# Optimization experiments

Hardware: AMD Instinct MI355X
Metric: run time of the kernel (lower is better)

The kernel has to match this reference:

```python
import jax, jax.numpy as jnp
import numpy as np

VIS_DIM, TXT_DIM, HID = 2048, 1024, 1024


def setup_inputs() -> dict:
    key = jax.random.key(0)
    ks = jax.random.split(key, 8)
    def lin(kw, kb, fan_in, fan_out):
        bound = 1.0 / np.sqrt(fan_in)
        W = jax.random.uniform(kw, (fan_out, fan_in), jnp.float32, -bound, bound)
        b = jax.random.uniform(kb, (fan_out,), jnp.float32, -bound, bound)
        return W, b
    Wv, bv = lin(ks[0], ks[1], VIS_DIM, HID)
    Wt, bt = lin(ks[2], ks[3], TXT_DIM, HID)
    Wa, ba = lin(ks[4], ks[5], HID, 1)
    return {
        "visual_features": jax.random.normal(ks[6], (128, 256, VIS_DIM), jnp.float32),
        "text_features": jax.random.normal(ks[7], (128, TXT_DIM), jnp.float32),
        "Wv": Wv, "bv": bv, "Wt": Wt, "bt": bt, "Wa": Wa, "ba": ba,
    }


def reference(visual_features, text_features, Wv, bv, Wt, bt, Wa, ba):
    # v: (B, R, H); t: (B, 1, H) broadcast over regions
    v = jnp.einsum("brd,hd->brh", visual_features, Wv) + bv
    t = (text_features @ Wt.T + bt)[:, None, :]
    combined = jnp.tanh(v + t)                       # (B, R, H)
    scores = jnp.einsum("brh,h->br", combined, Wa[0]) + ba[0]  # (B, R)
    attention_weights = jax.nn.softmax(scores, axis=1)
    attended = jnp.einsum("br,brd->bd", attention_weights, visual_features)
    return attended, attention_weights
```

## Files before the change

### kernel.cpp

```cpp
#include <hip/hip_runtime.h>
#include <hip/hip_bf16.h>

#define VIS_DIM 2048
#define TXT_DIM 1024
#define HID     1024
#define NB      128
#define NR      256
#define M_TOT   (NB*NR)

#define N_ATILES 8192
#define N_TILES  8448
#define TILE_B   16384
#define WS_SCORES_OFF ((size_t)N_TILES * TILE_B)
#define WS_NEED (WS_SCORES_OFF + 131072 + 524288)

typedef __attribute__((ext_vector_type(4))) float  f32x4;
typedef __attribute__((ext_vector_type(8))) short  short8;
typedef __attribute__((ext_vector_type(4))) unsigned short u16x4;

static __device__ __forceinline__ unsigned short f2bf(float f) {
    union { __hip_bfloat16 h; unsigned short u; } c;
    c.h = __float2bfloat16(f);
    return c.u;
}

static __device__ __forceinline__ float tanh_fast(float x) {
    float xc = fminf(fmaxf(x, -15.f), 15.f);
    float e  = __expf(2.f * xc);
    return (e - 1.f) / (e + 1.f);
}

__global__ void init_ws(float* __restrict__ scores, float* __restrict__ tbuf,
                        const float* __restrict__ bt) {
    int i = blockIdx.x * 256 + threadIdx.x;
    if (i < M_TOT) scores[i] = 0.f;
    tbuf[i] = bt[i & (HID - 1)];
}

__global__ __launch_bounds__(256) void prepass(const float* __restrict__ A,
                                               const float* __restrict__ Bv,
                                               unsigned short* __restrict__ w16) {
    const int t   = blockIdx.x;
    const int tid = threadIdx.x;
    const int mb  = (t < N_ATILES ? t : t - N_ATILES) >> 5;
    const int kt  = t & 31;
    const float* src = (t < N_ATILES ? A : Bv) + (size_t)mb * 128 * VIS_DIM + kt * 64;
    unsigned short* dst = w16 + (size_t)t * (TILE_B / 2);
    #pragma unroll
    for (int i = 0; i < 4; ++i) {
        int si = i * 256 + tid;
        int row = si >> 3, slot = si & 7;
        const float* p = src + (size_t)row * VIS_DIM + slot * 8;
        f32x4 lo = *(const f32x4*)p;
        f32x4 hi = *(const f32x4*)(p + 4);
        short8 v;
        v[0] = (short)f2bf(lo.x); v[1] = (short)f2bf(lo.y);
        v[2] = (short)f2bf(lo.z); v[3] = (short)f2bf(lo.w);
        v[4] = (short)f2bf(hi.x); v[5] = (short)f2bf(hi.y);
        v[6] = (short)f2bf(hi.z); v[7] = (short)f2bf(hi.w);
        *(short8*)(dst + row * 64 + ((slot ^ (row & 7)) << 3)) = v;
    }
}

__global__ __launch_bounds__(256) void gemm_text(const float* __restrict__ text,
                                                 const float* __restrict__ Wt,
                                                 float* __restrict__ tbuf) {
    __shared__ float As[128][33];
    __shared__ float Bs[32][33];
    const int n0  = blockIdx.x * 32;
    const int k0  = blockIdx.y * 256;
    const int tid = threadIdx.x;
    const int tm  = tid >> 3;
    const int tn  = tid & 7;
    float acc[4][4] = {};
    for (int kt = 0; kt < 8; ++kt) {
        const int k = k0 + kt * 32;
        {
            int row = tid >> 1, off = (tid & 1) * 16;
            const float* src = text + row * TXT_DIM + k + off;
            #pragma unroll
            for (int j = 0; j < 4; ++j) {
                f32x4 v = *(const f32x4*)(src + j * 4);
                As[row][off + j*4 + 0] = v.x; As[row][off + j*4 + 1] = v.y;
                As[row][off + j*4 + 2] = v.z; As[row][off + j*4 + 3] = v.w;
            }
        }
        {
            int row = tid >> 3, off = (tid & 7) * 4;
            f32x4 v = *(const f32x4*)(Wt + (size_t)(n0 + row) * TXT_DIM + k + off);
            Bs[row][off + 0] = v.x; Bs[row][off + 1] = v.y;
            Bs[row][off + 2] = v.z; Bs[row][off + 3] = v.w;
        }
        __syncthreads();
        #pragma unroll
        for (int kk = 0; kk < 32; ++kk) {
            float a[4], b[4];
            #pragma unroll
            for (int i = 0; i < 4; ++i) a[i] = As[tm*4 + i][kk];
            #pragma unroll
            for (int j = 0; j < 4; ++j) b[j] = Bs[tn*4 + j][kk];
            #pragma unroll
            for (int i = 0; i < 4; ++i)
                #pragma unroll
                for (int j = 0; j < 4; ++j) acc[i][j] += a[i] * b[j];
        }
        __syncthreads();
    }
    #pragma unroll
    for (int i = 0; i < 4; ++i)
        #pragma unroll
        for (int j = 0; j < 4; ++j)
            atomicAdd(&tbuf[(tm*4 + i) * HID + n0 + tn*4 + j], acc[i][j]);
}

static __device__ __forceinline__ int toff(int row, int kElem) {
    return row * 128 + ((((kElem >> 3) & 7) ^ (row & 7)) << 4);
}

__global__ __launch_bounds__(256, 3) void gemm_fast(
        const unsigned short* __restrict__ w16,
        const float* __restrict__ bv,
        const float* __restrict__ wa,
        const float* __restrict__ tbuf,
        float* __restrict__ scores) {
    __shared__ __align__(16) char lds[32768];

    const int wg   = blockIdx.x;
    const int xcd  = wg & 7;
    const int loc  = wg >> 3;
    const int mb   = xcd * 32 + (loc >> 3);
    const int nb   = loc & 7;
    const int brow = mb * 128;
    const int bcol = nb * 128;

    const int tid  = threadIdx.x;
    const int lane = tid & 63;
    const int wid  = tid >> 6;
    const int wr   = wid >> 1, wc = wid & 1;
    const int l    = lane & 15, g = lane >> 4;

    const char* Abase = (const char*)w16 + (size_t)(mb * 32) * TILE_B;
    const char* Bbase = (const char*)w16 + (size_t)(N_ATILES + nb * 32) * TILE_B;
    const int uoff = wid * 4096;

    f32x4 acc[4][4] = {};

    for (int kt = 0; kt < 32; ++kt) {
        const char* At = Abase + (size_t)kt * TILE_B;
        const char* Bt = Bbase + (size_t)kt * TILE_B;
        #pragma unroll
        for (int j = 0; j < 4; ++j) {
            const int off = uoff + j * 1024;
            __builtin_amdgcn_global_load_lds(
                (const __attribute__((address_space(1))) float*)(At + off + lane * 16),
                (__attribute__((address_space(3))) float*)(lds + off), 16, 0, 0);
            __builtin_amdgcn_global_load_lds(
                (const __attribute__((address_space(1))) float*)(Bt + off + lane * 16),
                (__attribute__((address_space(3))) float*)(lds + 16384 + off), 16, 0, 0);
        }
        __syncthreads();
        #pragma unroll
        for (int s = 0; s < 2; ++s) {
            short8 af[4], bf[4];
            const int kE = s * 32 + g * 8;
            #pragma unroll
            for (int m = 0; m < 4; ++m)
                af[m] = *(const short8*)(lds + toff(wr*64 + m*16 + l, kE));
            #pragma unroll
            for (int n = 0; n < 4; ++n)
                bf[n] = *(const short8*)(lds + 16384 + toff(wc*64 + n*16 + l, kE));
            #pragma unroll
            for (int m = 0; m < 4; ++m)
                #pragma unroll
                for (int n = 0; n < 4; ++n)
                    acc[m][n] = __builtin_amdgcn_mfma_f32_16x16x32_bf16(
                        af[m], bf[n], acc[m][n], 0, 0, 0);
        }
        __syncthreads();
    }

    const int b = brow >> 8;
    float wa_c[4], bvt_c[4];
    #pragma unroll
    for (int n = 0; n < 4; ++n) {
        int col = bcol + wc * 64 + n * 16 + l;
        wa_c[n]  = wa[col];
        bvt_c[n] = bv[col] + tbuf[b * HID + col];
    }
    #pragma unroll
    for (int m = 0; m < 4; ++m) {
        float p0 = 0.f, p1 = 0.f, p2 = 0.f, p3 = 0.f;
        #pragma unroll
        for (int n = 0; n < 4; ++n) {
            f32x4 v = acc[m][n];
            p0 += wa_c[n] * tanh_fast(v.x + bvt_c[n]);
            p1 += wa_c[n] * tanh_fast(v.y + bvt_c[n]);
            p2 += wa_c[n] * tanh_fast(v.z + bvt_c[n]);
            p3 += wa_c[n] * tanh_fast(v.w + bvt_c[n]);
        }
        #pragma unroll
        for (int d = 1; d < 16; d <<= 1) {
            p0 += __shfl_xor(p0, d); p1 += __shfl_xor(p1, d);
            p2 += __shfl_xor(p2, d); p3 += __shfl_xor(p3, d);
        }
        if ((lane & 15) == 0) {
            int rowg = brow + wr * 64 + m * 16 + (lane >> 4) * 4;
            atomicAdd(&scores[rowg + 0], p0);
            atomicAdd(&scores[rowg + 1], p1);
            atomicAdd(&scores[rowg + 2], p2);
            atomicAdd(&scores[rowg + 3], p3);
        }
    }
}

#define BK 32
#define NT (VIS_DIM / BK)

static __device__ __forceinline__ int tile_off(int row, int kElem) {
    return row * 64 + (((kElem >> 3) ^ ((row >> 1) & 3)) << 4);
}

__global__ __launch_bounds__(256, 2) void gemm_vis(
        const float* __restrict__ A,
        const float* __restrict__ Bv,
        const float* __restrict__ bv,
        const float* __restrict__ wa,
        const float* __restrict__ tbuf,
        float* __restrict__ scores) {
    __shared__ __align__(16) char lds[32768];

    const int wg   = blockIdx.x;
    const int xcd  = wg & 7;
    const int loc  = wg >> 3;
    const int mb   = xcd * 32 + (loc >> 3);
    const int nb   = loc & 7;
    const int brow = mb * 128;
    const int bcol = nb * 128;

    const int tid  = threadIdx.x;
    const int lane = tid & 63;
    const int wid  = tid >> 6;
    const int wr   = wid >> 1, wc = wid & 1;

    const int srow = tid >> 3;
    const int sfs  = tid & 7;
    unsigned va0 = ((unsigned)(brow + srow      ) * VIS_DIM + sfs * 4) * 4u;
    unsigned va1 = va0 + 32u * VIS_DIM * 4u;
    unsigned va2 = va0 + 64u * VIS_DIM * 4u;
    unsigned va3 = va0 + 96u * VIS_DIM * 4u;
    unsigned vb0 = ((unsigned)(bcol + srow      ) * VIS_DIM + sfs * 4) * 4u;
    unsigned vb1 = vb0 + 32u * VIS_DIM * 4u;
    unsigned vb2 = vb0 + 64u * VIS_DIM * 4u;
    unsigned vb3 = vb0 + 96u * VIS_DIM * 4u;

    int wbyte[4];
    #pragma unroll
    for (int r = 0; r < 4; ++r) {
        int row = srow + 32 * r;
        wbyte[r] = row * 64 + (((sfs >> 1) ^ ((row >> 1) & 3)) << 4) + (sfs & 1) * 8;
    }

    f32x4 sA0, sA1, sA2, sA3, sB0, sB1, sB2, sB3;
    f32x4 tA0, tA1, tA2, tA3, tB0, tB1, tB2, tB3;
    f32x4 acc[4][4] = {};

#define GLOAD_SET(dA0,dA1,dA2,dA3,dB0,dB1,dB2,dB3)                             \
    do {                                                                       \
        asm volatile("global_load_dwordx4 %0, %1, %2"                          \
                     : "=&v"(dA0) : "v"(va0), "s"(A) : "memory");              \
        asm volatile("global_load_dwordx4 %0, %1, %2"                          \
                     : "=&v"(dA1) : "v"(va1), "s"(A) : "memory");              \
        asm volatile("global_load_dwordx4 %0, %1, %2"                          \
                     : "=&v"(dA2) : "v"(va2), "s"(A) : "memory");              \
        asm volatile("global_load_dwordx4 %0, %1, %2"                          \
                     : "=&v"(dA3) : "v"(va3), "s"(A) : "memory");              \
        asm volatile("global_load_dwordx4 %0, %1, %2"                          \
                     : "=&v"(dB0) : "v"(vb0), "s"(Bv) : "memory");             \
        asm volatile("global_load_dwordx4 %0, %1, %2"                          \
                     : "=&v"(dB1) : "v"(vb1), "s"(Bv) : "memory");             \
        asm volatile("global_load_dwordx4 %0, %1, %2"                          \
                     : "=&v"(dB2) : "v"(vb2), "s"(Bv) : "memory");             \
        asm volatile("global_load_dwordx4 %0, %1, %2"                          \
                     : "=&v"(dB3) : "v"(vb3), "s"(Bv) : "memory");             \
        va0 += BK * 4; va1 += BK * 4; va2 += BK * 4; va3 += BK * 4;            \
        vb0 += BK * 4; vb1 += BK * 4; vb2 += BK * 4; vb3 += BK * 4;            \
    } while (0)

#define GLOAD_S() GLOAD_SET(sA0,sA1,sA2,sA3,sB0,sB1,sB2,sB3)
#define GLOAD_T() GLOAD_SET(tA0,tA1,tA2,tA3,tB0,tB1,tB2,tB3)

#define VWAIT(N)                                                               \
    do {                                                                       \
        __builtin_amdgcn_sched_barrier(0);                                     \
        asm volatile("s_waitcnt vmcnt(" #N ")" ::: "memory");                  \
        __builtin_amdgcn_sched_barrier(0);                                     \
    } while (0)

#define BARRIER()                                                              \
    do {                                                                       \
        __builtin_amdgcn_sched_barrier(0);                                     \
        asm volatile("s_waitcnt lgkmcnt(0)" ::: "memory");                     \
        __builtin_amdgcn_s_barrier();                                          \
        __builtin_amdgcn_sched_barrier(0);                                     \
    } while (0)

#define CVT8(dst, v0)                                                          \
    do {                                                                       \
        u16x4 t_;                                                              \
        t_.x = f2bf((v0).x); t_.y = f2bf((v0).y);                              \
        t_.z = f2bf((v0).z); t_.w = f2bf((v0).w);                              \
        dst = t_;                                                              \
    } while (0)

#define LWRITE_SET(bufbase, dA0,dA1,dA2,dA3,dB0,dB1,dB2,dB3)                   \
    do {                                                                       \
        u16x4 w_;                                                              \
        char* la = lds + (bufbase);                                            \
        char* lb = lds + (bufbase) + 8192;                                     \
        CVT8(w_, dA0); *(u16x4*)(la + wbyte[0]) = w_;                          \
        CVT8(w_, dA1); *(u16x4*)(la + wbyte[1]) = w_;                          \
        CVT8(w_, dA2); *(u16x4*)(la + wbyte[2]) = w_;                          \
        CVT8(w_, dA3); *(u16x4*)(la + wbyte[3]) = w_;                          \
        CVT8(w_, dB0); *(u16x4*)(lb + wbyte[0]) = w_;                          \
        CVT8(w_, dB1); *(u16x4*)(lb + wbyte[1]) = w_;                          \
        CVT8(w_, dB2); *(u16x4*)(lb + wbyte[2]) = w_;                          \
        CVT8(w_, dB3); *(u16x4*)(lb + wbyte[3]) = w_;                          \
    } while (0)

#define LWRITE_S(bufbase) LWRITE_SET(bufbase, sA0,sA1,sA2,sA3,sB0,sB1,sB2,sB3)
#define LWRITE_T(bufbase) LWRITE_SET(bufbase, tA0,tA1,tA2,tA3,tB0,tB1,tB2,tB3)

#define COMPUTE(bufbase)                                                       \
    do {                                                                       \
        short8 af[4], bf[4];                                                   \
        const int kk = (lane >> 4) * 8;                                        \
        const char* la = lds + (bufbase);                                      \
        const char* lb = lds + (bufbase) + 8192;                               \
        _Pragma("unroll")                                                      \
        for (int m = 0; m < 4; ++m)                                            \
            af[m] = *(const short8*)(la + tile_off(wr*64 + m*16 + (lane&15), kk)); \
        _Pragma("unroll")                                                      \
        for (int n = 0; n < 4; ++n)                                            \
            bf[n] = *(const short8*)(lb + tile_off(wc*64 + n*16 + (lane&15), kk)); \
        _Pragma("unroll")                                                      \
        for (int m = 0; m < 4; ++m)                                            \
            _Pragma("unroll")                                                  \
            for (int n = 0; n < 4; ++n)                                        \
                acc[m][n] = __builtin_amdgcn_mfma_f32_16x16x32_bf16(           \
                    af[m], bf[n], acc[m][n], 0, 0, 0);                         \
    } while (0)

    GLOAD_S();
    GLOAD_T();
    VWAIT(8);
    LWRITE_S(0);
    BARRIER();

    #pragma unroll 1
    for (int kt = 0; kt < NT - 2; kt += 2) {
        GLOAD_S();
        COMPUTE(0);
        VWAIT(8);
        LWRITE_T(16384);
        BARRIER();
        GLOAD_T();
        COMPUTE(16384);
        VWAIT(8);
        LWRITE_S(0);
        BARRIER();
    }
    COMPUTE(0);
    VWAIT(0);
    LWRITE_T(16384);
    BARRIER();
    COMPUTE(16384);
#undef GLOAD_SET
#undef GLOAD_S
#undef GLOAD_T
#undef VWAIT
#undef BARRIER
#undef CVT8
#undef LWRITE_SET
#undef LWRITE_S
#undef LWRITE_T
#undef COMPUTE

    const int b = brow >> 8;
    float wa_c[4], bvt_c[4];
    #pragma unroll
    for (int n = 0; n < 4; ++n) {
        int col = bcol + wc * 64 + n * 16 + (lane & 15);
        wa_c[n]  = wa[col];
        bvt_c[n] = bv[col] + tbuf[b * HID + col];
    }
    #pragma unroll
    for (int m = 0; m < 4; ++m) {
        float p0 = 0.f, p1 = 0.f, p2 = 0.f, p3 = 0.f;
        #pragma unroll
        for (int n = 0; n < 4; ++n) {
            f32x4 v = acc[m][n];
            p0 += wa_c[n] * tanh_fast(v.x + bvt_c[n]);
            p1 += wa_c[n] * tanh_fast(v.y + bvt_c[n]);
            p2 += wa_c[n] * tanh_fast(v.z + bvt_c[n]);
            p3 += wa_c[n] * tanh_fast(v.w + bvt_c[n]);
        }
        #pragma unroll
        for (int d = 1; d < 16; d <<= 1) {
            p0 += __shfl_xor(p0, d); p1 += __shfl_xor(p1, d);
            p2 += __shfl_xor(p2, d); p3 += __shfl_xor(p3, d);
        }
        if ((lane & 15) == 0) {
            int rowg = brow + wr * 64 + m * 16 + (lane >> 4) * 4;
            atomicAdd(&scores[rowg + 0], p0);
            atomicAdd(&scores[rowg + 1], p1);
            atomicAdd(&scores[rowg + 2], p2);
            atomicAdd(&scores[rowg + 3], p3);
        }
    }
}

__global__ __launch_bounds__(256) void attend(const float* __restrict__ visual,
                                              const float* __restrict__ scores,
                                              float* __restrict__ out) {
    const int chunk = blockIdx.x;
    const int b     = blockIdx.y;
    const int tid   = threadIdx.x;
    const int lane  = tid & 63;
    const int wv    = tid >> 6;

    __shared__ float wsm[NR];
    __shared__ float red[4];
    __shared__ f32x4 part[4][64];

    float s = scores[b * NR + tid];
    float mx = s;
    #pragma unroll
    for (int d = 1; d < 64; d <<= 1) mx = fmaxf(mx, __shfl_xor(mx, d));
    if (lane == 0) red[wv] = mx;
    __syncthreads();
    mx = fmaxf(fmaxf(red[0], red[1]), fmaxf(red[2], red[3]));
    float e = __expf(s - mx);
    float sum = e;
    #pragma unroll
    for (int d = 1; d < 64; d <<= 1) sum += __shfl_xor(sum, d);
    __syncthreads();
    if (lane == 0) red[wv] = sum;
    __syncthreads();
    sum = red[0] + red[1] + red[2] + red[3];
    float w = e * (1.f / sum);
    wsm[tid] = w;
    if (chunk == 0) out[(size_t)NB * VIS_DIM + b * NR + tid] = w;
    __syncthreads();

    const float* vb = visual + ((size_t)b * NR + wv * 64) * VIS_DIM + chunk * 256 + lane * 4;
    f32x4 acc = {0.f, 0.f, 0.f, 0.f};
    #pragma unroll
    for (int r = 0; r < 64; r += 4) {
        f32x4 v0 = *(const f32x4*)(vb + (size_t)(r + 0) * VIS_DIM);
        f32x4 v1 = *(const f32x4*)(vb + (size_t)(r + 1) * VIS_DIM);
        f32x4 v2 = *(const f32x4*)(vb + (size_t)(r + 2) * VIS_DIM);
        f32x4 v3 = *(const f32x4*)(vb + (size_t)(r + 3) * VIS_DIM);
        acc += wsm[wv * 64 + r + 0] * v0;
        acc += wsm[wv * 64 + r + 1] * v1;
        acc += wsm[wv * 64 + r + 2] * v2;
        acc += wsm[wv * 64 + r + 3] * v3;
    }
    part[wv][lane] = acc;
    __syncthreads();
    if (wv == 0) {
        f32x4 a = part[0][lane] + part[1][lane] + part[2][lane] + part[3][lane];
        *(f32x4*)(out + (size_t)b * VIS_DIM + chunk * 256 + lane * 4) = a;
    }
}

extern "C" void kernel_launch(void* const* d_in, const int* in_sizes, int n_in,
                              void* d_out, int out_size, void* d_ws, size_t ws_size,
                              hipStream_t stream) {
    (void)in_sizes; (void)n_in; (void)out_size;
    const float* visual = (const float*)d_in[0];
    const float* text   = (const float*)d_in[1];
    const float* Wv     = (const float*)d_in[2];
    const float* bv     = (const float*)d_in[3];
    const float* Wt     = (const float*)d_in[4];
    const float* bt     = (const float*)d_in[5];
    const float* Wa     = (const float*)d_in[6];

    float* out = (float*)d_out;
    const bool fast = ws_size >= (size_t)WS_NEED;

    if (fast) {
        unsigned short* w16 = (unsigned short*)d_ws;
        float* scores = (float*)((char*)d_ws + WS_SCORES_OFF);
        float* tbuf   = scores + M_TOT;
        prepass  <<<N_TILES, 256, 0, stream>>>(visual, Wv, w16);
        init_ws  <<<512, 256, 0, stream>>>(scores, tbuf, bt);
        gemm_text<<<dim3(32, 4), 256, 0, stream>>>(text, Wt, tbuf);
        gemm_fast<<<2048, 256, 0, stream>>>(w16, bv, Wa, tbuf, scores);
        attend   <<<dim3(8, NB), 256, 0, stream>>>(visual, scores, out);
    } else {
        float* scores = (float*)d_ws;
        float* tbuf   = scores + M_TOT;
        init_ws  <<<512, 256, 0, stream>>>(scores, tbuf, bt);
        gemm_text<<<dim3(32, 4), 256, 0, stream>>>(text, Wt, tbuf);
        gemm_vis <<<2048, 256, 0, stream>>>(visual, Wv, bv, Wa, tbuf, scores);
        attend   <<<dim3(8, NB), 256, 0, stream>>>(visual, scores, out);
    }
}
```

Measured before the change: 289.1 us.

## Enlarge GEMM tile to 256x256 with 8 waves and LDS double buffering

Replaces the 128x128 bf16 MFMA GEMM with a 256x256 tile computed by 512 threads (8 waves, each owning 128x64 of the output). Global-to-LDS loads are double-buffered across two 64KB halves, with explicit vmcnt/lgkmcnt waits and barriers, so loads of the next K step overlap MFMA work. The intent is to cut redundant global/L2 traffic per flop through higher operand reuse and to hide load latency. In exchange it uses 128KB of LDS and more accumulator registers per thread, which lowers occupancy, and it launches only 512 workgroups.

```diff
diff --git a/kernel.cpp b/kernel.cpp
--- a/kernel.cpp
+++ b/kernel.cpp
@@ -11,6 +11,7 @@
 #define N_ATILES 8192
 #define N_TILES  8448
 #define TILE_B   16384
+#define TSTRIDE  (32 * TILE_B)
 #define WS_SCORES_OFF ((size_t)N_TILES * TILE_B)
 #define WS_NEED (WS_SCORES_OFF + 131072 + 524288)
 
@@ -117,69 +118,113 @@
     return row * 128 + ((((kElem >> 3) & 7) ^ (row & 7)) << 4);
 }
 
-__global__ __launch_bounds__(256, 3) void gemm_fast(
+__global__ __launch_bounds__(512, 2) void gemm_256(
         const unsigned short* __restrict__ w16,
         const float* __restrict__ bv,
         const float* __restrict__ wa,
         const float* __restrict__ tbuf,
         float* __restrict__ scores) {
-    __shared__ __align__(16) char lds[32768];
+    __shared__ __align__(16) char lds[131072];
 
     const int wg   = blockIdx.x;
     const int xcd  = wg & 7;
     const int loc  = wg >> 3;
-    const int mb   = xcd * 32 + (loc >> 3);
-    const int nb   = loc & 7;
-    const int brow = mb * 128;
-    const int bcol = nb * 128;
+    const int mb   = xcd * 16 + (loc >> 2);
+    const int nb   = loc & 3;
+    const int brow = mb * 256;
+    const int bcol = nb * 256;
 
     const int tid  = threadIdx.x;
     const int lane = tid & 63;
     const int wid  = tid >> 6;
-    const int wr   = wid >> 1, wc = wid & 1;
+    const int wr   = wid >> 2;
+    const int wc   = wid & 3;
     const int l    = lane & 15, g = lane >> 4;
 
-    const char* Abase = (const char*)w16 + (size_t)(mb * 32) * TILE_B;
-    const char* Bbase = (const char*)w16 + (size_t)(N_ATILES + nb * 32) * TILE_B;
-    const int uoff = wid * 4096;
-
-    f32x4 acc[4][4] = {};
-
-    for (int kt = 0; kt < 32; ++kt) {
-        const char* At = Abase + (size_t)kt * TILE_B;
-        const char* Bt = Bbase + (size_t)kt * TILE_B;
-        #pragma unroll
-        for (int j = 0; j < 4; ++j) {
-            const int off = uoff + j * 1024;
-            __builtin_amdgcn_global_load_lds(
-                (const __attribute__((address_space(1))) float*)(At + off + lane * 16),
-                (__attribute__((address_space(3))) float*)(lds + off), 16, 0, 0);
-            __builtin_amdgcn_global_load_lds(
-                (const __attribute__((address_space(1))) float*)(Bt + off + lane * 16),
-                (__attribute__((address_space(3))) float*)(lds + 16384 + off), 16, 0, 0);
-        }
-        __syncthreads();
-        #pragma unroll
-        for (int s = 0; s < 2; ++s) {
-            short8 af[4], bf[4];
-            const int kE = s * 32 + g * 8;
-            #pragma unroll
-            for (int m = 0; m < 4; ++m)
-                af[m] = *(const short8*)(lds + toff(wr*64 + m*16 + l, kE));
-            #pragma unroll
-            for (int n = 0; n < 4; ++n)
-                bf[n] = *(const short8*)(lds + 16384 + toff(wc*64 + n*16 + l, kE));
-            #pragma unroll
-            for (int m = 0; m < 4; ++m)
-                #pragma unroll
-                for (int n = 0; n < 4; ++n)
-                    acc[m][n] = __builtin_amdgcn_mfma_f32_16x16x32_bf16(
-                        af[m], bf[n], acc[m][n], 0, 0, 0);
-        }
-        __syncthreads();
-    }
-
-    const int b = brow >> 8;
+    const char* wb = (const char*)w16;
+    const char* pA = wb + (size_t)(2 * mb) * TSTRIDE + wid * 1024 + lane * 16;
+    const char* pB = wb + (size_t)N_ATILES * TILE_B
+                        + (size_t)(2 * nb) * TSTRIDE + wid * 1024 + lane * 16;
+
+    f32x4 acc[8][4] = {};
+
+#define GLOADS(koff, bufbase)                                                  \
+    do {                                                                       \
+        _Pragma("unroll")                                                      \
+        for (int j = 0; j < 8; ++j) {                                          \
+            const char* s_ = (j < 4                                            \
+                ? pA + (j >> 1) * (size_t)TSTRIDE + (j & 1) * 8192             \
+                : pB + ((j - 4) >> 1) * (size_t)TSTRIDE + ((j - 4) & 1) * 8192)\
+                + (koff);                                                      \
+            __builtin_amdgcn_global_load_lds(                                  \
+                (const __attribute__((address_space(1))) float*)s_,            \
+                (__attribute__((address_space(3))) float*)                     \
+                    (lds + (bufbase) + j * 8192 + wid * 1024),                 \
+                16, 0, 0);                                                     \
+        }                                                                      \
+    } while (0)
+
+#define VWAIT0()                                                               \
+    do {                                                                       \
+        __builtin_amdgcn_sched_barrier(0);                                     \
+        asm volatile("s_waitcnt vmcnt(0)" ::: "memory");                       \
+        __builtin_amdgcn_sched_barrier(0);                                     \
+    } while (0)
+
+#define BARRIER()                                                              \
+    do {                                                                       \
+        __builtin_amdgcn_sched_barrier(0);                                     \
+        asm volatile("s_waitcnt lgkmcnt(0)" ::: "memory");                     \
+        __builtin_amdgcn_s_barrier();                                          \
+        __builtin_amdgcn_sched_barrier(0);                                     \
+    } while (0)
+
+#define PHASE(bufbase, s)                                                      \
+    do {                                                                       \
+        const int kE = (s) * 32 + g * 8;                                       \
+        const char* pa_ = lds + (bufbase) + wr * 16384;                        \
+        const char* pb_ = lds + (bufbase) + 32768 + (wc >> 1) * 16384;         \
+        short8 bfr[4];                                                         \
+        _Pragma("unroll")                                                      \
+        for (int n = 0; n < 4; ++n)                                            \
+            bfr[n] = *(const short8*)(pb_ + toff((wc & 1) * 64 + n * 16 + l, kE)); \
+        _Pragma("unroll")                                                      \
+        for (int m = 0; m < 8; ++m) {                                          \
+            short8 af = *(const short8*)(pa_ + toff(m * 16 + l, kE));          \
+            acc[m][0] = __builtin_amdgcn_mfma_f32_16x16x32_bf16(af, bfr[0], acc[m][0], 0, 0, 0); \
+            acc[m][1] = __builtin_amdgcn_mfma_f32_16x16x32_bf16(af, bfr[1], acc[m][1], 0, 0, 0); \
+            acc[m][2] = __builtin_amdgcn_mfma_f32_16x16x32_bf16(af, bfr[2], acc[m][2], 0, 0, 0); \
+            acc[m][3] = __builtin_amdgcn_mfma_f32_16x16x32_bf16(af, bfr[3], acc[m][3], 0, 0, 0); \
+        }                                                                      \
+    } while (0)
+
+    GLOADS((size_t)0, 0);
+    VWAIT0();
+    GLOADS((size_t)TILE_B, 65536);
+    BARRIER();
+
+    #pragma unroll 1
+    for (int i = 0; i < 16; ++i) {
+        const size_t k2 = (size_t)(2 * i + 2) * TILE_B;
+        PHASE(0, 0);
+        PHASE(0, 1);
+        VWAIT0();
+        BARRIER();
+        if (i < 15) GLOADS(k2, 0);
+        PHASE(65536, 0);
+        PHASE(65536, 1);
+        if (i < 15) {
+            VWAIT0();
+            BARRIER();
+            GLOADS(k2 + TILE_B, 65536);
+        }
+    }
+#undef GLOADS
+#undef VWAIT0
+#undef BARRIER
+#undef PHASE
+
+    const int b = mb;
     float wa_c[4], bvt_c[4];
     #pragma unroll
     for (int n = 0; n < 4; ++n) {
@@ -188,7 +233,7 @@
         bvt_c[n] = bv[col] + tbuf[b * HID + col];
     }
     #pragma unroll
-    for (int m = 0; m < 4; ++m) {
+    for (int m = 0; m < 8; ++m) {
         float p0 = 0.f, p1 = 0.f, p2 = 0.f, p3 = 0.f;
         #pragma unroll
         for (int n = 0; n < 4; ++n) {
@@ -204,7 +249,7 @@
             p2 += __shfl_xor(p2, d); p3 += __shfl_xor(p3, d);
         }
         if ((lane & 15) == 0) {
-            int rowg = brow + wr * 64 + m * 16 + (lane >> 4) * 4;
+            int rowg = brow + wr * 128 + m * 16 + g * 4;
             atomicAdd(&scores[rowg + 0], p0);
             atomicAdd(&scores[rowg + 1], p1);
             atomicAdd(&scores[rowg + 2], p2);
@@ -495,7 +540,7 @@
         prepass  <<<N_TILES, 256, 0, stream>>>(visual, Wv, w16);
         init_ws  <<<512, 256, 0, stream>>>(scores, tbuf, bt);
         gemm_text<<<dim3(32, 4), 256, 0, stream>>>(text, Wt, tbuf);
-        gemm_fast<<<2048, 256, 0, stream>>>(w16, bv, Wa, tbuf, scores);
+        gemm_256 <<<512, 512, 0, stream>>>(w16, bv, Wa, tbuf, scores);
         attend   <<<dim3(8, NB), 256, 0, stream>>>(visual, scores, out);
     } else {
         float* scores = (float*)d_ws;
```

New measurement: 270.7 us. 1.07x faster.
